# Performance work log

Hardware: AMD Instinct MI355X
Metric: run time of the kernel (lower is better)

## Reference

```python
import jax, jax.numpy as jnp
import numpy as np

NUM_BITS = 4
BLOCK = 64
OUT_F, IN_F = 4096, 4096
RANK = 16


def _uniform_table():
    # BlockQuantizer.create_uniform_map(symmetric=False, num_bits=4)
    return jnp.linspace(-1.0, 1.0, 2 ** NUM_BITS).astype(jnp.float32)


def _dequantize(qweight, weight_max):
    """Unpack 4-bit codes (2 per byte), lookup codebook, apply per-64 block scale.
    qweight: [OUT*IN/2, 1] int32 in [0,256); weight_max: [OUT*IN/64, 1] float32.
    Returns [OUT_F, IN_F] float32."""
    table = _uniform_table()
    q = qweight[:, 0]
    idx_lo = q & 15          # packed at shift 0
    idx_hi = (q >> 4) & 15   # packed at shift 4
    w = jnp.stack([table[idx_lo], table[idx_hi]], axis=-1)  # [N/2, 2]
    w = w.reshape(-1, BLOCK) * weight_max                   # per-block scale
    return w.reshape(OUT_F, IN_F)


def setup_inputs() -> dict:
    key = jax.random.key(0)
    k1, k2, k3, k4, k5, k6 = jax.random.split(key, 6)
    x = jax.random.normal(k1, (4, 2048, IN_F), dtype=jnp.float32)
    qweight = jax.random.randint(k2, (OUT_F * IN_F // 2, 1), 0, 256, dtype=jnp.int32)
    weight_max = jax.random.uniform(k3, (OUT_F * IN_F // BLOCK, 1), dtype=jnp.float32,
                                    minval=0.01, maxval=1.0)
    lora_A = jax.random.normal(k4, (RANK, IN_F), dtype=jnp.float32) * 0.02
    lora_B = jax.random.normal(k5, (OUT_F, RANK), dtype=jnp.float32) * 0.02
    bias = jax.random.normal(k6, (OUT_F,), dtype=jnp.float32) * 0.02
    return {"x": x, "qweight": qweight, "weight_max": weight_max,
            "lora_A": lora_A, "lora_B": lora_B, "bias": bias}


def reference(x, qweight, weight_max, lora_A, lora_B, bias):
    # Dequantize block-quantized base weight, then linear + LoRA correction.
    W = _dequantize(qweight, weight_max)                     # [out, in]
    y = jnp.einsum('bsi,oi->bso', x, W) + bias               # base linear
    a = jnp.einsum('bsi,ri->bsr', x, lora_A)                 # lora_A(x)
    y = y + jnp.einsum('bsr,or->bso', a, lora_B)             # + lora_B(.)
    return y
```

## Files before the change

kernel.cpp:

```cpp
#include <hip/hip_runtime.h>
#include <hip/hip_bf16.h>
#include <stdint.h>

typedef __bf16 bf16_t;
typedef bf16_t bf16x8 __attribute__((ext_vector_type(8)));
typedef float f32x4 __attribute__((ext_vector_type(4)));

#define IN_F 4096
#define OUT_F 4096
#define M_ROWS 8192
#define RANK 16

__global__ __launch_bounds__(256)
void dequant_lora_kernel(const int* __restrict__ qw, const float* __restrict__ wmax,
                         const float* __restrict__ lA, const float* __restrict__ lB,
                         bf16_t* __restrict__ Wp) {
  const int tid = blockIdx.x * 256 + threadIdx.x;
  const int f0 = tid * 8;
  const int o  = f0 >> 12;
  const int i0 = f0 & (IN_F - 1);
  const int4 q4 = *(const int4*)(qw + (f0 >> 1));
  const float scale = wmax[f0 >> 6];
  const float st = scale * (2.0f / 15.0f);

  float v[8];
  {
    const int q0 = q4.x, q1 = q4.y, q2 = q4.z, q3 = q4.w;
    v[0] = (float)(q0 & 15)        * st - scale;
    v[1] = (float)((q0 >> 4) & 15) * st - scale;
    v[2] = (float)(q1 & 15)        * st - scale;
    v[3] = (float)((q1 >> 4) & 15) * st - scale;
    v[4] = (float)(q2 & 15)        * st - scale;
    v[5] = (float)((q2 >> 4) & 15) * st - scale;
    v[6] = (float)(q3 & 15)        * st - scale;
    v[7] = (float)((q3 >> 4) & 15) * st - scale;
  }

  const float* Brow = lB + o * RANK;
#pragma unroll
  for (int r = 0; r < RANK; ++r) {
    const float br = Brow[r];
    const float4 a0 = *(const float4*)(lA + r * IN_F + i0);
    const float4 a1 = *(const float4*)(lA + r * IN_F + i0 + 4);
    v[0] += br * a0.x; v[1] += br * a0.y; v[2] += br * a0.z; v[3] += br * a0.w;
    v[4] += br * a1.x; v[5] += br * a1.y; v[6] += br * a1.z; v[7] += br * a1.w;
  }

  bf16x8 ov;
#pragma unroll
  for (int j = 0; j < 8; ++j) ov[j] = (bf16_t)v[j];
  *(bf16x8*)(Wp + (size_t)f0) = ov;
}

__global__ __launch_bounds__(256)
void f32_to_bf16_kernel(const float* __restrict__ x, bf16_t* __restrict__ xb) {
  const size_t tid = (size_t)blockIdx.x * 256 + threadIdx.x;
  const float4 a0 = *(const float4*)(x + tid * 8);
  const float4 a1 = *(const float4*)(x + tid * 8 + 4);
  bf16x8 o;
  o[0] = (bf16_t)a0.x; o[1] = (bf16_t)a0.y; o[2] = (bf16_t)a0.z; o[3] = (bf16_t)a0.w;
  o[4] = (bf16_t)a1.x; o[5] = (bf16_t)a1.y; o[6] = (bf16_t)a1.z; o[7] = (bf16_t)a1.w;
  *(bf16x8*)(xb + tid * 8) = o;
}

__device__ __forceinline__ void gld(const bf16_t* src, char* dst) {
  __builtin_amdgcn_global_load_lds((const __attribute__((address_space(1))) void*)src,
                                   (__attribute__((address_space(3))) void*)dst, 16, 0, 0);
}

#define BARRIER() __builtin_amdgcn_s_barrier()
#define WAIT_LGKM0() do { asm volatile("s_waitcnt lgkmcnt(0)" ::: "memory"); \
                          __builtin_amdgcn_sched_barrier(0); } while (0)
#define WAIT_VM(n) asm volatile("s_waitcnt vmcnt(" #n ")" ::: "memory")

#define LDA(buf, m, cb) (*(const bf16x8*)(ldsA + ((buf)*32768 + aRowB + (m)*2048 + (cb))))
#define LDB(buf, n, cb) (*(const bf16x8*)(ldsB + ((buf)*32768 + bRowB + (n)*2048 + (cb))))

#define STAGE_A(kt, buf) do { \
  _Pragma("unroll") for (int g = 0; g < 4; ++g) \
    gld(Asrc + ((size_t)g*64*IN_F + (size_t)(kt)*64), ldsA + ((buf)*32768 + g*8192 + tid*16)); \
} while (0)
#define STAGE_B_HALF(kt, buf, h) do { \
  _Pragma("unroll") for (int g = 0; g < 2; ++g) \
    gld(Bsrc + ((size_t)((h)*2+g)*64*IN_F + (size_t)(kt)*64), \
        ldsB + ((buf)*32768 + ((h)*2+g)*8192 + tid*16)); \
} while (0)
#define STAGE_B(kt, buf) do { STAGE_B_HALF(kt, buf, 0); STAGE_B_HALF(kt, buf, 1); } while (0)

#define READ_B_ALL(buf) do { \
  _Pragma("unroll") for (int n = 0; n < 4; ++n) { \
    b[n][0] = LDB(buf, n, cA0); b[n][1] = LDB(buf, n, cA1); } \
} while (0)

#define PHASE(Q, EXTRA, STAGE, TAILWAIT) do { \
  a[0][0] = LDA(cur, 2*(Q),   cA0); a[0][1] = LDA(cur, 2*(Q),   cA1); \
  a[1][0] = LDA(cur, 2*(Q)+1, cA0); a[1][1] = LDA(cur, 2*(Q)+1, cA1); \
  EXTRA; STAGE; \
  BARRIER(); \
  WAIT_LGKM0(); \
  __builtin_amdgcn_s_setprio(1); \
  _Pragma("unroll") for (int kh = 0; kh < 2; ++kh) \
    _Pragma("unroll") for (int mm = 0; mm < 2; ++mm) \
      _Pragma("unroll") for (int n = 0; n < 4; ++n) \
        acc[2*(Q)+mm][n] = __builtin_amdgcn_mfma_f32_16x16x32_bf16( \
            a[mm][kh], b[n][kh], acc[2*(Q)+mm][n], 0, 0, 0); \
  __builtin_amdgcn_s_setprio(0); \
  TAILWAIT; \
  BARRIER(); \
} while (0)

__global__ __launch_bounds__(512, 2)
void gemm_8phase_kernel(const bf16_t* __restrict__ Xb, const bf16_t* __restrict__ Wp,
                        const float* __restrict__ bias, float* __restrict__ C) {
  __shared__ __align__(16) bf16_t As[2][256][64];
  __shared__ __align__(16) bf16_t Bs[2][256][64];
  char* ldsA = (char*)As;
  char* ldsB = (char*)Bs;

  const int tid  = threadIdx.x;
  const int lane = tid & 63;
  const int wave = tid >> 6;
  const int wr = wave >> 2;
  const int wc = wave & 3;
  const int r16 = lane & 15;
  const int kg  = lane >> 4;

  const int bid = blockIdx.x;
  const int bm = bid >> 4;
  const int bn = bid & 15;

  const int sr = tid >> 3;
  const int sc = ((tid & 7) ^ (sr & 7)) << 3;
  const bf16_t* Asrc = Xb + (size_t)(bm * 256 + sr) * IN_F + sc;
  const bf16_t* Bsrc = Wp + (size_t)(bn * 256 + sr) * IN_F + sc;

  const int aRowB = (wr * 128 + r16) * 128;
  const int bRowB = (wc * 64 + r16) * 128;
  const int cA0 = (kg * 16) ^ ((r16 & 7) << 4);
  const int cA1 = cA0 ^ 64;

  f32x4 acc[8][4] = {};
  bf16x8 a[2][2], b[4][2];

  STAGE_A(0, 0); STAGE_B(0, 0);
  STAGE_A(1, 1); STAGE_B(1, 1);
  WAIT_VM(8);
  BARRIER();

  for (int t = 0; t < 64; ++t) {
    const int cur = t & 1;
    PHASE(0, READ_B_ALL(cur),
          { if (t >= 1 && t < 63) STAGE_A(t + 1, cur ^ 1); }, {});
    PHASE(1, {},
          { if (t < 62) STAGE_B_HALF(t + 2, cur, 0); }, {});
    PHASE(2, {},
          { if (t < 62) STAGE_B_HALF(t + 2, cur, 1); }, {});
    PHASE(3, {}, {},
          { if (t < 62) { WAIT_VM(4); } else if (t == 62) { WAIT_VM(0); } });
  }

#pragma unroll
  for (int n = 0; n < 4; ++n) {
    const int col = bn * 256 + wc * 64 + n * 16 + r16;
    const float bv = bias[col];
#pragma unroll
    for (int m = 0; m < 8; ++m) {
      const int row0 = bm * 256 + wr * 128 + m * 16 + kg * 4;
#pragma unroll
      for (int r = 0; r < 4; ++r)
        C[(size_t)(row0 + r) * OUT_F + col] = acc[m][n][r] + bv;
    }
  }
}

extern "C" void kernel_launch(void* const* d_in, const int* in_sizes, int n_in,
                              void* d_out, int out_size, void* d_ws, size_t ws_size,
                              hipStream_t stream) {
  const float* x  = (const float*)d_in[0];
  const int*   qw = (const int*)d_in[1];
  const float* wm = (const float*)d_in[2];
  const float* lA = (const float*)d_in[3];
  const float* lB = (const float*)d_in[4];
  const float* bs = (const float*)d_in[5];
  float* out = (float*)d_out;

  bf16_t* Wp = (bf16_t*)d_ws;
  bf16_t* Xb = (bf16_t*)((char*)d_ws + (size_t)OUT_F * IN_F * 2);

  dequant_lora_kernel<<<OUT_F * IN_F / 8 / 256, 256, 0, stream>>>(qw, wm, lA, lB, Wp);
  f32_to_bf16_kernel<<<M_ROWS * IN_F / 8 / 256, 256, 0, stream>>>(x, Xb);
  gemm_8phase_kernel<<<(M_ROWS / 256) * (OUT_F / 256), 512, 0, stream>>>(Xb, Wp, bs, out);
}
```

Measured before the change: 347.7 us.

## Split A-tile staging into per-phase quarters with finer vmcnt waits

Reorganises the A tile in LDS into four row-quarters, one per compute phase, so that each phase only needs its own quarter of A. This lets the loads for the next tiles be spread across all four phases of the GEMM main loop instead of being issued in bulk. Each phase now waits on a tuned vmcnt count, and the last two k-tiles are peeled into an explicit epilogue. The aim is smoother overlap of global-to-LDS loads with MFMA work. The cost is fragile hand-counted wait values that could cause races if any count is wrong.

```diff
diff --git a/kernel.cpp b/kernel.cpp
--- a/kernel.cpp
+++ b/kernel.cpp
@@ -73,29 +73,29 @@
                           __builtin_amdgcn_sched_barrier(0); } while (0)
 #define WAIT_VM(n) asm volatile("s_waitcnt vmcnt(" #n ")" ::: "memory")
 
-#define LDA(buf, m, cb) (*(const bf16x8*)(ldsA + ((buf)*32768 + aRowB + (m)*2048 + (cb))))
-#define LDB(buf, n, cb) (*(const bf16x8*)(ldsB + ((buf)*32768 + bRowB + (n)*2048 + (cb))))
-
-#define STAGE_A(kt, buf) do { \
-  _Pragma("unroll") for (int g = 0; g < 4; ++g) \
-    gld(Asrc + ((size_t)g*64*IN_F + (size_t)(kt)*64), ldsA + ((buf)*32768 + g*8192 + tid*16)); \
+#define STAGE_AQ(kt, buf, q) \
+  gld(AsrcQ + (size_t)(q) * 32 * IN_F + (size_t)(kt) * 64, \
+      ldsA + (buf) * 32768 + (q) * 8192 + tid * 16)
+#define STAGE_BH(kt, buf, h) do { \
+  gld(Bsrc + (size_t)((h)*2)   * 64 * IN_F + (size_t)(kt) * 64, \
+      ldsB + (buf) * 32768 + ((h)*2)   * 8192 + tid * 16); \
+  gld(Bsrc + (size_t)((h)*2+1) * 64 * IN_F + (size_t)(kt) * 64, \
+      ldsB + (buf) * 32768 + ((h)*2+1) * 8192 + tid * 16); \
 } while (0)
-#define STAGE_B_HALF(kt, buf, h) do { \
-  _Pragma("unroll") for (int g = 0; g < 2; ++g) \
-    gld(Bsrc + ((size_t)((h)*2+g)*64*IN_F + (size_t)(kt)*64), \
-        ldsB + ((buf)*32768 + ((h)*2+g)*8192 + tid*16)); \
-} while (0)
-#define STAGE_B(kt, buf) do { STAGE_B_HALF(kt, buf, 0); STAGE_B_HALF(kt, buf, 1); } while (0)
-
-#define READ_B_ALL(buf) do { \
-  _Pragma("unroll") for (int n = 0; n < 4; ++n) { \
-    b[n][0] = LDB(buf, n, cA0); b[n][1] = LDB(buf, n, cA1); } \
-} while (0)
-
-#define PHASE(Q, EXTRA, STAGE, TAILWAIT) do { \
-  a[0][0] = LDA(cur, 2*(Q),   cA0); a[0][1] = LDA(cur, 2*(Q),   cA1); \
-  a[1][0] = LDA(cur, 2*(Q)+1, cA0); a[1][1] = LDA(cur, 2*(Q)+1, cA1); \
-  EXTRA; STAGE; \
+
+#define LDA(buf, q, mm, cb) \
+  (*(const bf16x8*)(ldsA + (buf)*32768 + (q)*8192 + aRowB + (mm)*2048 + (cb)))
+#define LDB(buf, n, cb) \
+  (*(const bf16x8*)(ldsB + (buf)*32768 + bRowB + (n)*2048 + (cb)))
+
+#define PH(Q, CUR, RDB, STG, TW) do { \
+  a[0][0] = LDA(CUR, Q, 0, cA0); a[0][1] = LDA(CUR, Q, 0, cA1); \
+  a[1][0] = LDA(CUR, Q, 1, cA0); a[1][1] = LDA(CUR, Q, 1, cA1); \
+  if (RDB) { \
+    _Pragma("unroll") for (int n = 0; n < 4; ++n) { \
+      b[n][0] = LDB(CUR, n, cA0); b[n][1] = LDB(CUR, n, cA1); } \
+  } \
+  STG; \
   BARRIER(); \
   WAIT_LGKM0(); \
   __builtin_amdgcn_s_setprio(1); \
@@ -105,15 +105,15 @@
         acc[2*(Q)+mm][n] = __builtin_amdgcn_mfma_f32_16x16x32_bf16( \
             a[mm][kh], b[n][kh], acc[2*(Q)+mm][n], 0, 0, 0); \
   __builtin_amdgcn_s_setprio(0); \
-  TAILWAIT; \
+  TW; \
   BARRIER(); \
 } while (0)
 
 __global__ __launch_bounds__(512, 2)
 void gemm_8phase_kernel(const bf16_t* __restrict__ Xb, const bf16_t* __restrict__ Wp,
                         const float* __restrict__ bias, float* __restrict__ C) {
-  __shared__ __align__(16) bf16_t As[2][256][64];
-  __shared__ __align__(16) bf16_t Bs[2][256][64];
+  __shared__ __align__(16) bf16_t As[2 * 16384];
+  __shared__ __align__(16) bf16_t Bs[2 * 16384];
   char* ldsA = (char*)As;
   char* ldsB = (char*)Bs;
 
@@ -129,12 +129,13 @@
   const int bm = bid >> 4;
   const int bn = bid & 15;
 
-  const int sr = tid >> 3;
-  const int sc = ((tid & 7) ^ (sr & 7)) << 3;
-  const bf16_t* Asrc = Xb + (size_t)(bm * 256 + sr) * IN_F + sc;
-  const bf16_t* Bsrc = Wp + (size_t)(bn * 256 + sr) * IN_F + sc;
-
-  const int aRowB = (wr * 128 + r16) * 128;
+  const int lr = tid >> 3;
+  const int sc = ((tid & 7) ^ (lr & 7)) << 3;
+  const int arow = (lr < 32) ? lr : (96 + lr);
+  const bf16_t* AsrcQ = Xb + (size_t)(bm * 256 + arow) * IN_F + sc;
+  const bf16_t* Bsrc  = Wp + (size_t)(bn * 256 + lr) * IN_F + sc;
+
+  const int aRowB = (wr * 32 + r16) * 128;
   const int bRowB = (wc * 64 + r16) * 128;
   const int cA0 = (kg * 16) ^ ((r16 & 7) << 4);
   const int cA1 = cA0 ^ 64;
@@ -142,22 +143,30 @@
   f32x4 acc[8][4] = {};
   bf16x8 a[2][2], b[4][2];
 
-  STAGE_A(0, 0); STAGE_B(0, 0);
-  STAGE_A(1, 1); STAGE_B(1, 1);
-  WAIT_VM(8);
+  STAGE_AQ(0, 0, 0);
+  STAGE_BH(0, 0, 0); STAGE_BH(0, 0, 1);
+  STAGE_AQ(0, 0, 1); STAGE_AQ(0, 0, 2); STAGE_AQ(0, 0, 3);
+  STAGE_BH(1, 1, 0); STAGE_AQ(1, 1, 0);
+  STAGE_BH(1, 1, 1); STAGE_AQ(1, 1, 1);
+  STAGE_AQ(1, 1, 2);
+  WAIT_VM(10);
   BARRIER();
 
-  for (int t = 0; t < 64; ++t) {
+  for (int t = 0; t < 62; ++t) {
     const int cur = t & 1;
-    PHASE(0, READ_B_ALL(cur),
-          { if (t >= 1 && t < 63) STAGE_A(t + 1, cur ^ 1); }, {});
-    PHASE(1, {},
-          { if (t < 62) STAGE_B_HALF(t + 2, cur, 0); }, {});
-    PHASE(2, {},
-          { if (t < 62) STAGE_B_HALF(t + 2, cur, 1); }, {});
-    PHASE(3, {}, {},
-          { if (t < 62) { WAIT_VM(4); } else if (t == 62) { WAIT_VM(0); } });
-  }
+    PH(0, cur, 1, { STAGE_AQ(t + 1, cur ^ 1, 3); },                      WAIT_VM(10));
+    PH(1, cur, 0, { STAGE_BH(t + 2, cur, 0); STAGE_AQ(t + 2, cur, 0); }, WAIT_VM(12));
+    PH(2, cur, 0, { STAGE_BH(t + 2, cur, 1); STAGE_AQ(t + 2, cur, 1); }, WAIT_VM(14));
+    PH(3, cur, 0, { STAGE_AQ(t + 2, cur, 2); },                          WAIT_VM(10));
+  }
+  PH(0, 0, 1, { STAGE_AQ(63, 1, 3); }, WAIT_VM(10));
+  PH(1, 0, 0, {},                      WAIT_VM(9));
+  PH(2, 0, 0, {},                      WAIT_VM(8));
+  PH(3, 0, 0, {},                      WAIT_VM(3));
+  PH(0, 1, 1, {},                      WAIT_VM(2));
+  PH(1, 1, 0, {},                      WAIT_VM(1));
+  PH(2, 1, 0, {},                      WAIT_VM(0));
+  PH(3, 1, 0, {},                      {});
 
 #pragma unroll
   for (int n = 0; n < 4; ++n) {
```

New measurement: 351.0 us. About the same (+0.9%).

## Restructure GEMM main loop into register double-buffered LDS-fragment pipeline

Applied to the files above, without the earlier changes.

Replaces the 8-phase loop, which had two barriers per phase and a full lgkmcnt wait before each MFMA group, with a software pipeline. A fragments for the next quarter are loaded from LDS while the current quarter's MFMAs run. B fragments for the next K tile are prefetched into alternating register sets, and global-to-LDS staging for tile t+2 is issued once per tile after a single barrier. This cuts barriers and exposed LDS latency per tile, at the cost of more fragment registers, which adds register pressure under the 2-block occupancy bound. It also relies on compiler-inserted waits for LDS reads, since the explicit lgkmcnt waits are removed.

```diff
diff --git a/kernel.cpp b/kernel.cpp
--- a/kernel.cpp
+++ b/kernel.cpp
@@ -69,51 +69,66 @@
 }
 
 #define BARRIER() __builtin_amdgcn_s_barrier()
-#define WAIT_LGKM0() do { asm volatile("s_waitcnt lgkmcnt(0)" ::: "memory"); \
-                          __builtin_amdgcn_sched_barrier(0); } while (0)
+#define SBAR()    __builtin_amdgcn_sched_barrier(0)
 #define WAIT_VM(n) asm volatile("s_waitcnt vmcnt(" #n ")" ::: "memory")
 
 #define LDA(buf, m, cb) (*(const bf16x8*)(ldsA + ((buf)*32768 + aRowB + (m)*2048 + (cb))))
 #define LDB(buf, n, cb) (*(const bf16x8*)(ldsB + ((buf)*32768 + bRowB + (n)*2048 + (cb))))
 
-#define STAGE_A(kt, buf) do { \
+#define STAGE_A4(kt, buf) do { \
   _Pragma("unroll") for (int g = 0; g < 4; ++g) \
     gld(Asrc + ((size_t)g*64*IN_F + (size_t)(kt)*64), ldsA + ((buf)*32768 + g*8192 + tid*16)); \
 } while (0)
-#define STAGE_B_HALF(kt, buf, h) do { \
-  _Pragma("unroll") for (int g = 0; g < 2; ++g) \
-    gld(Bsrc + ((size_t)((h)*2+g)*64*IN_F + (size_t)(kt)*64), \
-        ldsB + ((buf)*32768 + ((h)*2+g)*8192 + tid*16)); \
-} while (0)
-#define STAGE_B(kt, buf) do { STAGE_B_HALF(kt, buf, 0); STAGE_B_HALF(kt, buf, 1); } while (0)
-
-#define READ_B_ALL(buf) do { \
+#define STAGE_B4(kt, buf) do { \
+  _Pragma("unroll") for (int g = 0; g < 4; ++g) \
+    gld(Bsrc + ((size_t)g*64*IN_F + (size_t)(kt)*64), ldsB + ((buf)*32768 + g*8192 + tid*16)); \
+} while (0)
+
+#define LOADA2(dst, m0, buf) do { \
+  dst[0][0] = LDA(buf, m0,     cA0); dst[0][1] = LDA(buf, m0,     cA1); \
+  dst[1][0] = LDA(buf, (m0)+1, cA0); dst[1][1] = LDA(buf, (m0)+1, cA1); \
+} while (0)
+
+#define PREFETCH12(buf, BFN) do { \
+  LOADA2(aF0, 0, buf); \
   _Pragma("unroll") for (int n = 0; n < 4; ++n) { \
-    b[n][0] = LDB(buf, n, cA0); b[n][1] = LDB(buf, n, cA1); } \
-} while (0)
-
-#define PHASE(Q, EXTRA, STAGE, TAILWAIT) do { \
-  a[0][0] = LDA(cur, 2*(Q),   cA0); a[0][1] = LDA(cur, 2*(Q),   cA1); \
-  a[1][0] = LDA(cur, 2*(Q)+1, cA0); a[1][1] = LDA(cur, 2*(Q)+1, cA1); \
-  EXTRA; STAGE; \
-  BARRIER(); \
-  WAIT_LGKM0(); \
+    BFN[n][0] = LDB(buf, n, cA0); BFN[n][1] = LDB(buf, n, cA1); } \
+} while (0)
+
+#define MFMA_Q(Q, AF, BF) do { \
+  SBAR(); \
   __builtin_amdgcn_s_setprio(1); \
   _Pragma("unroll") for (int kh = 0; kh < 2; ++kh) \
-    _Pragma("unroll") for (int mm = 0; mm < 2; ++mm) \
-      _Pragma("unroll") for (int n = 0; n < 4; ++n) \
-        acc[2*(Q)+mm][n] = __builtin_amdgcn_mfma_f32_16x16x32_bf16( \
-            a[mm][kh], b[n][kh], acc[2*(Q)+mm][n], 0, 0, 0); \
+  _Pragma("unroll") for (int mm = 0; mm < 2; ++mm) \
+  _Pragma("unroll") for (int n = 0; n < 4; ++n) \
+    acc[2*(Q)+mm][n] = __builtin_amdgcn_mfma_f32_16x16x32_bf16( \
+        AF[mm][kh], BF[n][kh], acc[2*(Q)+mm][n], 0, 0, 0); \
   __builtin_amdgcn_s_setprio(0); \
-  TAILWAIT; \
-  BARRIER(); \
+} while (0)
+
+#define TILE(CUR, BFC, BFN, tv) do { \
+   \
+  LOADA2(aF1, 2, CUR); \
+  MFMA_Q(0, aF0, BFC); \
+   \
+  LOADA2(aF0, 4, CUR); \
+  MFMA_Q(1, aF1, BFC); \
+  if ((tv) < 63) { SBAR(); WAIT_VM(0); BARRIER(); SBAR(); } \
+   \
+  LOADA2(aF1, 6, CUR); \
+  MFMA_Q(2, aF0, BFC); \
+  if ((tv) < 63) { SBAR(); PREFETCH12((CUR) ^ 1, BFN); SBAR(); } \
+   \
+  MFMA_Q(3, aF1, BFC); \
+  if ((tv) < 62) { SBAR(); BARRIER(); SBAR(); \
+                   STAGE_A4((tv) + 2, CUR); STAGE_B4((tv) + 2, CUR); SBAR(); } \
 } while (0)
 
 __global__ __launch_bounds__(512, 2)
-void gemm_8phase_kernel(const bf16_t* __restrict__ Xb, const bf16_t* __restrict__ Wp,
-                        const float* __restrict__ bias, float* __restrict__ C) {
-  __shared__ __align__(16) bf16_t As[2][256][64];
-  __shared__ __align__(16) bf16_t Bs[2][256][64];
+void gemm_pipe_kernel(const bf16_t* __restrict__ Xb, const bf16_t* __restrict__ Wp,
+                      const float* __restrict__ bias, float* __restrict__ C) {
+  __shared__ __align__(16) bf16_t As[2 * 16384];
+  __shared__ __align__(16) bf16_t Bs[2 * 16384];
   char* ldsA = (char*)As;
   char* ldsB = (char*)Bs;
 
@@ -140,23 +155,17 @@
   const int cA1 = cA0 ^ 64;
 
   f32x4 acc[8][4] = {};
-  bf16x8 a[2][2], b[4][2];
-
-  STAGE_A(0, 0); STAGE_B(0, 0);
-  STAGE_A(1, 1); STAGE_B(1, 1);
+  bf16x8 aF0[2][2], aF1[2][2], bFe[4][2], bFo[4][2];
+
+  STAGE_A4(0, 0); STAGE_B4(0, 0);
+  STAGE_A4(1, 1); STAGE_B4(1, 1);
   WAIT_VM(8);
-  BARRIER();
-
-  for (int t = 0; t < 64; ++t) {
-    const int cur = t & 1;
-    PHASE(0, READ_B_ALL(cur),
-          { if (t >= 1 && t < 63) STAGE_A(t + 1, cur ^ 1); }, {});
-    PHASE(1, {},
-          { if (t < 62) STAGE_B_HALF(t + 2, cur, 0); }, {});
-    PHASE(2, {},
-          { if (t < 62) STAGE_B_HALF(t + 2, cur, 1); }, {});
-    PHASE(3, {}, {},
-          { if (t < 62) { WAIT_VM(4); } else if (t == 62) { WAIT_VM(0); } });
+  BARRIER(); SBAR();
+  PREFETCH12(0, bFe);
+
+  for (int tt = 0; tt < 64; tt += 2) {
+    TILE(0, bFe, bFo, tt);
+    TILE(1, bFo, bFe, tt + 1);
   }
 
 #pragma unroll
@@ -189,5 +198,5 @@
 
   dequant_lora_kernel<<<OUT_F * IN_F / 8 / 256, 256, 0, stream>>>(qw, wm, lA, lB, Wp);
   f32_to_bf16_kernel<<<M_ROWS * IN_F / 8 / 256, 256, 0, stream>>>(x, Xb);
-  gemm_8phase_kernel<<<(M_ROWS / 256) * (OUT_F / 256), 512, 0, stream>>>(Xb, Wp, bs, out);
-}
+  gemm_pipe_kernel<<<(M_ROWS / 256) * (OUT_F / 256), 512, 0, stream>>>(Xb, Wp, bs, out);
+}
```

Result: slower. 381.9 us (+9.8%).

## Change LDS swizzle, remap GEMM workgroups per XCD, and tile dequant blocks

Applied to the files above, without the earlier changes.

The GEMM kernel gets a different LDS swizzle: the XOR now flips bit 4 of the column based on the row pair, and the row offsets are rearranged to match. This is meant to cut LDS bank conflicts on the MFMA operand reads. Workgroup IDs are remapped so that consecutive blocks placed on the same XCD share A/B tiles, aiming for better L2 reuse. The dequant kernel now gives each block an 8-row by 256-column tile so that lora_A columns are reused across rows, with the risk that the new swizzle mapping is wrong for some lanes.

```diff
diff --git a/kernel.cpp b/kernel.cpp
--- a/kernel.cpp
+++ b/kernel.cpp
@@ -15,10 +15,14 @@
 void dequant_lora_kernel(const int* __restrict__ qw, const float* __restrict__ wmax,
                          const float* __restrict__ lA, const float* __restrict__ lB,
                          bf16_t* __restrict__ Wp) {
-  const int tid = blockIdx.x * 256 + threadIdx.x;
-  const int f0 = tid * 8;
-  const int o  = f0 >> 12;
-  const int i0 = f0 & (IN_F - 1);
+  const int bid = blockIdx.x;
+  const int bo = bid >> 4;
+  const int bi = bid & 15;
+  const int t  = threadIdx.x;
+  const int o  = bo * 8 + (t >> 5);
+  const int i0 = bi * 256 + (t & 31) * 8;
+  const int f0 = o * IN_F + i0;
+
   const int4 q4 = *(const int4*)(qw + (f0 >> 1));
   const float scale = wmax[f0 >> 6];
   const float st = scale * (2.0f / 15.0f);
@@ -89,12 +93,12 @@
 
 #define READ_B_ALL(buf) do { \
   _Pragma("unroll") for (int n = 0; n < 4; ++n) { \
-    b[n][0] = LDB(buf, n, cA0); b[n][1] = LDB(buf, n, cA1); } \
+    b[n][0] = LDB(buf, n, cS0); b[n][1] = LDB(buf, n, cS1); } \
 } while (0)
 
 #define PHASE(Q, EXTRA, STAGE, TAILWAIT) do { \
-  a[0][0] = LDA(cur, 2*(Q),   cA0); a[0][1] = LDA(cur, 2*(Q),   cA1); \
-  a[1][0] = LDA(cur, 2*(Q)+1, cA0); a[1][1] = LDA(cur, 2*(Q)+1, cA1); \
+  a[0][0] = LDA(cur, 2*(Q),   cS0); a[0][1] = LDA(cur, 2*(Q),   cS1); \
+  a[1][0] = LDA(cur, 2*(Q)+1, cS0); a[1][1] = LDA(cur, 2*(Q)+1, cS1); \
   EXTRA; STAGE; \
   BARRIER(); \
   WAIT_LGKM0(); \
@@ -110,10 +114,10 @@
 } while (0)
 
 __global__ __launch_bounds__(512, 2)
-void gemm_8phase_kernel(const bf16_t* __restrict__ Xb, const bf16_t* __restrict__ Wp,
-                        const float* __restrict__ bias, float* __restrict__ C) {
-  __shared__ __align__(16) bf16_t As[2][256][64];
-  __shared__ __align__(16) bf16_t Bs[2][256][64];
+void gemm_m201_kernel(const bf16_t* __restrict__ Xb, const bf16_t* __restrict__ Wp,
+                      const float* __restrict__ bias, float* __restrict__ C) {
+  __shared__ __align__(16) bf16_t As[2 * 16384];
+  __shared__ __align__(16) bf16_t Bs[2 * 16384];
   char* ldsA = (char*)As;
   char* ldsB = (char*)Bs;
 
@@ -125,19 +129,20 @@
   const int r16 = lane & 15;
   const int kg  = lane >> 4;
 
-  const int bid = blockIdx.x;
-  const int bm = bid >> 4;
-  const int bn = bid & 15;
+  const int bid  = blockIdx.x;
+  const int wgid = (bid & 7) * 64 + (bid >> 3);
+  const int bm = wgid >> 4;
+  const int bn = wgid & 15;
 
-  const int sr = tid >> 3;
-  const int sc = ((tid & 7) ^ (sr & 7)) << 3;
-  const bf16_t* Asrc = Xb + (size_t)(bm * 256 + sr) * IN_F + sc;
-  const bf16_t* Bsrc = Wp + (size_t)(bn * 256 + sr) * IN_F + sc;
+  const int srow = tid >> 3;
+  const int scol = ((tid & 7) * 8) ^ (((tid >> 5) & 1) << 4);
+  const bf16_t* Asrc = Xb + (size_t)(bm * 256 + srow) * IN_F + scol;
+  const bf16_t* Bsrc = Wp + (size_t)(bn * 256 + srow) * IN_F + scol;
 
-  const int aRowB = (wr * 128 + r16) * 128;
-  const int bRowB = (wc * 64 + r16) * 128;
-  const int cA0 = (kg * 16) ^ ((r16 & 7) << 4);
-  const int cA1 = cA0 ^ 64;
+  const int aRowB = wr * 16384 + r16 * 128;
+  const int bRowB = (wc >> 1) * 16384 + (wc & 1) * 8192 + r16 * 128;
+  const int cS0 = (kg * 16) ^ ((r16 & 4) << 3);
+  const int cS1 = cS0 + 64;
 
   f32x4 acc[8][4] = {};
   bf16x8 a[2][2], b[4][2];
@@ -187,7 +192,7 @@
   bf16_t* Wp = (bf16_t*)d_ws;
   bf16_t* Xb = (bf16_t*)((char*)d_ws + (size_t)OUT_F * IN_F * 2);
 
-  dequant_lora_kernel<<<OUT_F * IN_F / 8 / 256, 256, 0, stream>>>(qw, wm, lA, lB, Wp);
+  dequant_lora_kernel<<<8192, 256, 0, stream>>>(qw, wm, lA, lB, Wp);
   f32_to_bf16_kernel<<<M_ROWS * IN_F / 8 / 256, 256, 0, stream>>>(x, Xb);
-  gemm_8phase_kernel<<<(M_ROWS / 256) * (OUT_F / 256), 512, 0, stream>>>(Xb, Wp, bs, out);
+  gemm_m201_kernel<<<(M_ROWS / 256) * (OUT_F / 256), 512, 0, stream>>>(Xb, Wp, bs, out);
 }
```

New measurement: 329.8 us. 1.05x faster.
